# Kernel optimization log

Measured on AMD Instinct MI355X. Metric: run time of the kernel, lower is better.

## Reference

```python
import jax, jax.numpy as jnp
import numpy as np

D_K = 64
EPS = 1e-6


def setup_inputs() -> dict:
    key = jax.random.key(0)
    ks = jax.random.split(key, 6)
    B, S, D2, DV = 4, 2048, 1024, 64
    q = jax.random.normal(ks[0], (B, S, D2), dtype=jnp.float32)
    k = jax.random.normal(ks[1], (B, S, D2), dtype=jnp.float32)
    v = jax.random.normal(ks[2], (B, S, D2), dtype=jnp.float32)
    mask = jax.random.randint(ks[3], (B, S, S), 0, 2) == 1
    V = jax.random.normal(ks[4], (1, DV), dtype=jnp.float32)
    fc_w = jax.random.normal(ks[5], (D2, DV), dtype=jnp.float32) * (1.0 / np.sqrt(DV))
    fc_b = jnp.zeros((D2,), dtype=jnp.float32)
    ln_g = jnp.ones((D2,), dtype=jnp.float32)
    ln_b = jnp.zeros((D2,), dtype=jnp.float32)
    return {"q": q, "k": k, "v": v, "mask": mask, "V": V,
            "fc_w": fc_w, "fc_b": fc_b, "ln_g": ln_g, "ln_b": ln_b}


def _layer_norm(x, g, b):
    mu = jnp.mean(x, axis=-1, keepdims=True)
    var = jnp.var(x, axis=-1, keepdims=True)
    return (x - mu) * jax.lax.rsqrt(var + EPS) * g + b


def reference(q, k, v, mask, V, fc_w, fc_b, ln_g, ln_b):
    residual = q
    qn = _layer_norm(q, ln_g, ln_b)
    # scaled dot-product scores (no softmax in this variant)
    attn = jnp.einsum('bsd,btd->bst', qn / jnp.sqrt(jnp.float32(D_K)), k)
    attn = jnp.where(mask, 0.0, attn)  # masked_fill with 0
    # v_ = V broadcast over (batch, seq, key); attn @ v_ == row-sum outer V
    output = jnp.sum(attn, axis=-1, keepdims=True) * V  # [B,S,d_v]
    output = output @ fc_w.T + fc_b                     # [B,S,2*d_model]
    output = output + residual
    return (output, attn)
```

## Files before the change

kernel.cpp:

```cpp
#include <hip/hip_runtime.h>
#include <hip/hip_bf16.h>
#include <cstdint>

#define S_LEN 2048
#define D2_   1024
#define DV_   64
#define NB_   4

typedef __bf16 bf16x8 __attribute__((ext_vector_type(8)));
typedef float  f32x4  __attribute__((ext_vector_type(4)));

__device__ __forceinline__ unsigned short f2bf(float f) {
  union { float f; unsigned int u; } v; v.f = f;
  unsigned int r = v.u + 0x7fffu + ((v.u >> 16) & 1u);
  return (unsigned short)(r >> 16);
}

__device__ __forceinline__ void async16(const unsigned short* g, unsigned short* l) {
  __builtin_amdgcn_global_load_lds(
      (__attribute__((address_space(1))) void*)g,
      (__attribute__((address_space(3))) void*)l,
      16, 0, 0);
}

__global__ void __launch_bounds__(256) prep_kernel(
    const float* __restrict__ q, const float* __restrict__ k,
    const float* __restrict__ gam, const float* __restrict__ bet,
    const float* __restrict__ V, const float* __restrict__ fw,
    unsigned short* __restrict__ qn, unsigned short* __restrict__ kb,
    float* __restrict__ w2, float* __restrict__ rowsum) {
  const int row = blockIdx.x;
  const int t = threadIdx.x;

  if (row < 32) rowsum[row * 256 + t] = 0.0f;

  const float4 x = ((const float4*)(q + (size_t)row * D2_))[t];
  float s  = x.x + x.y + x.z + x.w;
  float ss = x.x * x.x + x.y * x.y + x.z * x.z + x.w * x.w;
  #pragma unroll
  for (int o = 32; o > 0; o >>= 1) { s += __shfl_down(s, o); ss += __shfl_down(ss, o); }
  __shared__ float red[8];
  if ((t & 63) == 0) { red[t >> 6] = s; red[(t >> 6) + 4] = ss; }
  __syncthreads();
  const float tot  = red[0] + red[1] + red[2] + red[3];
  const float tots = red[4] + red[5] + red[6] + red[7];
  const float mu  = tot * (1.0f / D2_);
  const float var = tots * (1.0f / D2_) - mu * mu;
  const float rs  = rsqrtf(var + 1e-6f) * 0.125f;
  const float4 gv = ((const float4*)gam)[t];
  const float4 bv = ((const float4*)bet)[t];
  ushort4 o4;
  o4.x = f2bf((x.x - mu) * rs * gv.x + 0.125f * bv.x);
  o4.y = f2bf((x.y - mu) * rs * gv.y + 0.125f * bv.y);
  o4.z = f2bf((x.z - mu) * rs * gv.z + 0.125f * bv.z);
  o4.w = f2bf((x.w - mu) * rs * gv.w + 0.125f * bv.w);
  ((ushort4*)(qn + (size_t)row * D2_))[t] = o4;

  const float4 kx = ((const float4*)(k + (size_t)row * D2_))[t];
  ushort4 k4;
  k4.x = f2bf(kx.x); k4.y = f2bf(kx.y); k4.z = f2bf(kx.z); k4.w = f2bf(kx.w);
  ((ushort4*)(kb + (size_t)row * D2_))[t] = k4;

  if (row < 4) {
    const int d = row * 256 + t;
    const float4* r  = (const float4*)(fw + (size_t)d * DV_);
    const float4* vv = (const float4*)V;
    float acc = 0.f;
    #pragma unroll
    for (int j = 0; j < 16; ++j) {
      const float4 a = r[j], b = vv[j];
      acc += a.x * b.x + a.y * b.y + a.z * b.z + a.w * b.w;
    }
    w2[d] = acc;
  }
}

__global__ void __launch_bounds__(512, 4) attn_gemm_kernel(
    const unsigned short* __restrict__ qn,
    const unsigned short* __restrict__ kb,
    const int* __restrict__ mask,
    float* __restrict__ attn,
    float* __restrict__ rowsum) {
  __shared__ __align__(16) unsigned short Asm_[2 * 8192];
  __shared__ __align__(16) unsigned short Bsm_[2 * 8192];

  const int t = threadIdx.x;

  const int orig = blockIdx.x + 16 * (blockIdx.y + 16 * blockIdx.z);
  const int swz  = (orig & 7) * 128 + (orig >> 3);
  const int bn = (swz & 15) * 128;
  const int bm = ((swz >> 4) & 15) * 128;
  const int bt = swz >> 8;

  const int srow_ = t >> 3;
  const int pg_   = (t & 7) ^ (srow_ & 7);
  const unsigned short* gA = qn + ((size_t)bt * S_LEN + bm + srow_) * D2_ + pg_ * 8;
  const unsigned short* gB = kb + ((size_t)bt * S_LEN + bn + srow_) * D2_ + pg_ * 8;
  unsigned short* lA = Asm_ + t * 8;
  unsigned short* lB = Bsm_ + t * 8;

  const int lane = t & 63;
  const int w  = t >> 6;
  const int wm = (w >> 2) * 64;
  const int wn = (w & 3) * 32;
  const int lr = lane & 15;
  const int lg = lane >> 4;

  #define STAGE64(buf, koff) do {                                   \
      async16(gA + (koff),            lA + (buf));                  \
      async16(gA + (koff) + 64 * D2_, lA + (buf) + 4096);           \
      async16(gB + (koff),            lB + (buf));                  \
      async16(gB + (koff) + 64 * D2_, lB + (buf) + 4096);           \
    } while (0)

  STAGE64(0, 0);

  const int m_base = bm + wm + lr;
  const size_t rb0 = ((size_t)bt * S_LEN) * S_LEN;
  int4 mk[4][2];
  #pragma unroll
  for (int fm = 0; fm < 4; ++fm)
    #pragma unroll
    for (int fn = 0; fn < 2; ++fn)
      mk[fm][fn] = *(const int4*)(mask + rb0 + (size_t)(m_base + fm * 16) * S_LEN
                                  + bn + wn + fn * 16 + lg * 4);

  f32x4 acc[4][2] = {};

  auto compute = [&](int pl) {
    #pragma unroll
    for (int ks = 0; ks < 2; ++ks) {
      const int sl = ((ks << 2) + lg) ^ (lr & 7);
      bf16x8 af[4], bfv[2];
      #pragma unroll
      for (int f = 0; f < 4; ++f)
        af[f]  = *(const bf16x8*)(Asm_ + pl + (wm + f * 16 + lr) * 64 + sl * 8);
      #pragma unroll
      for (int f = 0; f < 2; ++f)
        bfv[f] = *(const bf16x8*)(Bsm_ + pl + (wn + f * 16 + lr) * 64 + sl * 8);
      #pragma unroll
      for (int fm = 0; fm < 4; ++fm)
        #pragma unroll
        for (int fn = 0; fn < 2; ++fn)
          acc[fm][fn] = __builtin_amdgcn_mfma_f32_16x16x32_bf16(
              bfv[fn], af[fm], acc[fm][fn], 0, 0, 0);
    }
  };

  __syncthreads();

  #pragma unroll 1
  for (int kt = 0; kt < 14; kt += 2) {
    STAGE64(8192, (kt + 1) * 64);
    compute(0);
    __syncthreads();
    STAGE64(0, (kt + 2) * 64);
    compute(8192);
    __syncthreads();
  }
  STAGE64(8192, 15 * 64);
  compute(0);
  __syncthreads();
  compute(8192);

  #pragma unroll
  for (int fm = 0; fm < 4; ++fm) {
    const int m = m_base + fm * 16;
    const size_t rowbase = rb0 + (size_t)m * S_LEN;
    float s = 0.f;
    #pragma unroll
    for (int fn = 0; fn < 2; ++fn) {
      const int n0 = bn + wn + fn * 16 + lg * 4;
      f32x4 v;
      v[0] = mk[fm][fn].x ? 0.0f : acc[fm][fn][0];
      v[1] = mk[fm][fn].y ? 0.0f : acc[fm][fn][1];
      v[2] = mk[fm][fn].z ? 0.0f : acc[fm][fn][2];
      v[3] = mk[fm][fn].w ? 0.0f : acc[fm][fn][3];
      __builtin_nontemporal_store(v, (f32x4*)(attn + rowbase + n0));
      s += v[0] + v[1] + v[2] + v[3];
    }
    s += __shfl_xor(s, 16);
    s += __shfl_xor(s, 32);
    if (lane < 16) atomicAdd(rowsum + (size_t)bt * S_LEN + m, s);
  }
  #undef STAGE64
}

__global__ void __launch_bounds__(256) out_kernel(
    const float* __restrict__ rowsum, const float* __restrict__ q,
    const float* __restrict__ w2, const float* __restrict__ fcb,
    float* __restrict__ out) {
  const int row = blockIdx.x;
  const int t = threadIdx.x;
  const float rs = rowsum[row];
  const float4 wv = ((const float4*)w2)[t];
  const float4 bv = ((const float4*)fcb)[t];
  const float4 qv = ((const float4*)(q + (size_t)row * D2_))[t];
  float4 o4;
  o4.x = rs * wv.x + bv.x + qv.x;
  o4.y = rs * wv.y + bv.y + qv.y;
  o4.z = rs * wv.z + bv.z + qv.z;
  o4.w = rs * wv.w + bv.w + qv.w;
  ((float4*)(out + (size_t)row * D2_))[t] = o4;
}

extern "C" void kernel_launch(void* const* d_in, const int* in_sizes, int n_in,
                              void* d_out, int out_size, void* d_ws, size_t ws_size,
                              hipStream_t stream) {
  (void)in_sizes; (void)n_in; (void)out_size; (void)ws_size;
  const float* q    = (const float*)d_in[0];
  const float* k    = (const float*)d_in[1];
  const int*   mask = (const int*)d_in[3];
  const float* V    = (const float*)d_in[4];
  const float* fw   = (const float*)d_in[5];
  const float* fcb  = (const float*)d_in[6];
  const float* lg   = (const float*)d_in[7];
  const float* lb   = (const float*)d_in[8];

  float* out  = (float*)d_out;
  float* attn = out + (size_t)NB_ * S_LEN * D2_;

  unsigned short* qn = (unsigned short*)out;
  unsigned short* kb = qn + (size_t)NB_ * S_LEN * D2_;
  float* w2     = (float*)d_ws;
  float* rowsum = w2 + D2_;

  prep_kernel<<<NB_ * S_LEN, 256, 0, stream>>>(q, k, lg, lb, V, fw, qn, kb, w2, rowsum);
  attn_gemm_kernel<<<dim3(S_LEN / 128, S_LEN / 128, NB_), 512, 0, stream>>>(qn, kb, mask, attn, rowsum);
  out_kernel<<<NB_ * S_LEN, 256, 0, stream>>>(rowsum, q, w2, fcb, out);
}
```

Before: 271.0 us.

## Single-buffer GEMM tiles and defer mask loads to raise occupancy

Replaces the double-buffered LDS staging with a single buffer, so each K step loads and then waits with barriers instead of overlapping copy and compute. The launch bound rises from 4 to 8 waves per SIMD. Mask values are now loaded nontemporally in the epilogue instead of being held in registers for the whole K loop. The attn store becomes a regular store instead of nontemporal. The aim is more resident blocks to hide latency through occupancy, at the cost of losing explicit load/compute overlap and adding a sync per stage.

After: 269.8 us. Within noise of the previous version (-0.4%).

```diff
diff --git a/kernel.cpp b/kernel.cpp
--- a/kernel.cpp
+++ b/kernel.cpp
@@ -9,6 +9,7 @@
 
 typedef __bf16 bf16x8 __attribute__((ext_vector_type(8)));
 typedef float  f32x4  __attribute__((ext_vector_type(4)));
+typedef int    i32x4  __attribute__((ext_vector_type(4)));
 
 __device__ __forceinline__ unsigned short f2bf(float f) {
   union { float f; unsigned int u; } v; v.f = f;
@@ -75,14 +76,14 @@
   }
 }
 
-__global__ void __launch_bounds__(512, 4) attn_gemm_kernel(
+__global__ void __launch_bounds__(512, 8) attn_gemm_kernel(
     const unsigned short* __restrict__ qn,
     const unsigned short* __restrict__ kb,
     const int* __restrict__ mask,
     float* __restrict__ attn,
     float* __restrict__ rowsum) {
-  __shared__ __align__(16) unsigned short Asm_[2 * 8192];
-  __shared__ __align__(16) unsigned short Bsm_[2 * 8192];
+  __shared__ __align__(16) unsigned short Asm_[8192];
+  __shared__ __align__(16) unsigned short Bsm_[8192];
 
   const int t = threadIdx.x;
 
@@ -106,38 +107,30 @@
   const int lr = lane & 15;
   const int lg = lane >> 4;
 
-  #define STAGE64(buf, koff) do {                                   \
-      async16(gA + (koff),            lA + (buf));                  \
-      async16(gA + (koff) + 64 * D2_, lA + (buf) + 4096);           \
-      async16(gB + (koff),            lB + (buf));                  \
-      async16(gB + (koff) + 64 * D2_, lB + (buf) + 4096);           \
+  #define STAGE(koff) do {                                    \
+      async16(gA + (koff),            lA);                    \
+      async16(gA + (koff) + 64 * D2_, lA + 4096);             \
+      async16(gB + (koff),            lB);                    \
+      async16(gB + (koff) + 64 * D2_, lB + 4096);             \
     } while (0)
 
-  STAGE64(0, 0);
-
-  const int m_base = bm + wm + lr;
-  const size_t rb0 = ((size_t)bt * S_LEN) * S_LEN;
-  int4 mk[4][2];
-  #pragma unroll
-  for (int fm = 0; fm < 4; ++fm)
-    #pragma unroll
-    for (int fn = 0; fn < 2; ++fn)
-      mk[fm][fn] = *(const int4*)(mask + rb0 + (size_t)(m_base + fm * 16) * S_LEN
-                                  + bn + wn + fn * 16 + lg * 4);
-
   f32x4 acc[4][2] = {};
 
-  auto compute = [&](int pl) {
+  STAGE(0);
+  __syncthreads();
+
+  #pragma unroll 1
+  for (int kt = 0; kt < 16; ++kt) {
     #pragma unroll
     for (int ks = 0; ks < 2; ++ks) {
       const int sl = ((ks << 2) + lg) ^ (lr & 7);
       bf16x8 af[4], bfv[2];
       #pragma unroll
       for (int f = 0; f < 4; ++f)
-        af[f]  = *(const bf16x8*)(Asm_ + pl + (wm + f * 16 + lr) * 64 + sl * 8);
+        af[f]  = *(const bf16x8*)(Asm_ + (wm + f * 16 + lr) * 64 + sl * 8);
       #pragma unroll
       for (int f = 0; f < 2; ++f)
-        bfv[f] = *(const bf16x8*)(Bsm_ + pl + (wn + f * 16 + lr) * 64 + sl * 8);
+        bfv[f] = *(const bf16x8*)(Bsm_ + (wn + f * 16 + lr) * 64 + sl * 8);
       #pragma unroll
       for (int fm = 0; fm < 4; ++fm)
         #pragma unroll
@@ -145,24 +138,15 @@
           acc[fm][fn] = __builtin_amdgcn_mfma_f32_16x16x32_bf16(
               bfv[fn], af[fm], acc[fm][fn], 0, 0, 0);
     }
-  };
-
-  __syncthreads();
-
-  #pragma unroll 1
-  for (int kt = 0; kt < 14; kt += 2) {
-    STAGE64(8192, (kt + 1) * 64);
-    compute(0);
     __syncthreads();
-    STAGE64(0, (kt + 2) * 64);
-    compute(8192);
-    __syncthreads();
+    if (kt < 15) {
+      STAGE((kt + 1) * 64);
+      __syncthreads();
+    }
   }
-  STAGE64(8192, 15 * 64);
-  compute(0);
-  __syncthreads();
-  compute(8192);
-
+
+  const int m_base = bm + wm + lr;
+  const size_t rb0 = ((size_t)bt * S_LEN) * S_LEN;
   #pragma unroll
   for (int fm = 0; fm < 4; ++fm) {
     const int m = m_base + fm * 16;
@@ -171,19 +155,20 @@
     #pragma unroll
     for (int fn = 0; fn < 2; ++fn) {
       const int n0 = bn + wn + fn * 16 + lg * 4;
+      const i32x4 mk = __builtin_nontemporal_load((const i32x4*)(mask + rowbase + n0));
       f32x4 v;
-      v[0] = mk[fm][fn].x ? 0.0f : acc[fm][fn][0];
-      v[1] = mk[fm][fn].y ? 0.0f : acc[fm][fn][1];
-      v[2] = mk[fm][fn].z ? 0.0f : acc[fm][fn][2];
-      v[3] = mk[fm][fn].w ? 0.0f : acc[fm][fn][3];
-      __builtin_nontemporal_store(v, (f32x4*)(attn + rowbase + n0));
+      v[0] = mk[0] ? 0.0f : acc[fm][fn][0];
+      v[1] = mk[1] ? 0.0f : acc[fm][fn][1];
+      v[2] = mk[2] ? 0.0f : acc[fm][fn][2];
+      v[3] = mk[3] ? 0.0f : acc[fm][fn][3];
+      *(f32x4*)(attn + rowbase + n0) = v;
       s += v[0] + v[1] + v[2] + v[3];
     }
     s += __shfl_xor(s, 16);
     s += __shfl_xor(s, 32);
     if (lane < 16) atomicAdd(rowsum + (size_t)bt * S_LEN + m, s);
   }
-  #undef STAGE64
+  #undef STAGE
 }
 
 __global__ void __launch_bounds__(256) out_kernel(
```
